# Kernel optimization log

Hardware: AMD Instinct MI355X
Metric: run time of the kernel (lower is better)

The kernel has to match this reference:

```python
import jax, jax.numpy as jnp
import numpy as np

B, N, D = 256, 131072, 256
TEMP = 0.05
EPS_SM = 1e-6
EPS_LOG = 1e-6
NUM_CLUSTERS = 1000


def _l2norm(x):
    return x / jnp.linalg.norm(x, axis=-1, keepdims=True)


def setup_inputs() -> dict:
    key = jax.random.key(0)
    k1, k2, k3, k4, k5 = jax.random.split(key, 5)
    # re-ID features are L2-normalized in practice; keeps exp(logits/temp) finite
    inputs = _l2norm(jax.random.normal(k1, (B, D), jnp.float32))
    indexes = jax.random.randint(k2, (B,), 0, N)
    labels = jax.random.randint(k3, (N,), 0, NUM_CLUSTERS)  # pseudo cluster ids buffer
    cluster_features = _l2norm(jax.random.normal(k4, (N, D), jnp.float32))
    instance_features = _l2norm(jax.random.normal(k5, (N, D), jnp.float32))
    return {
        "inputs": inputs,
        "cluster_features": cluster_features,
        "instance_features": instance_features,
        "indexes": indexes,
        "labels": labels,
    }


def reference(inputs, cluster_features, instance_features, indexes, labels):
    # targets = labels[indexes]
    targets = labels[indexes]
    # bank similarity GEMM, temperature scaling
    logits = jnp.matmul(inputs, cluster_features.T) / TEMP  # [B, N]
    # module's custom softmax: exp / (sum + eps)  (intentionally no max-subtract)
    exps = jnp.exp(logits)
    masked_sim = exps / (jnp.sum(exps, axis=1, keepdims=True) + EPS_SM)
    logp = jnp.log(masked_sim + EPS_LOG)
    # F.nll_loss: mean of -logp at target column
    loss = -jnp.mean(jnp.take_along_axis(logp, targets[:, None], axis=1))
    return loss
```

## Files before the change

kernel.cpp:

```cpp
#include <hip/hip_runtime.h>
#include <hip/hip_bf16.h>
#include <cstdint>

#define B_ 256
#define N_ 131072
#define D_ 256
#define INV_TEMP 20.0f
#define EPS_SM 1e-6f
#define EPS_LOG 1e-6f

#define TPB 512
#define BN 128
#define BK 64
#define TILES 4
#define LDB 72
#define BUFE (BN * LDB)
#define NSLOT 32

typedef __bf16 bf16_t;
typedef bf16_t bf16x8 __attribute__((ext_vector_type(8)));
typedef float f32x4 __attribute__((ext_vector_type(4)));

__device__ inline ushort f2bf(float f) {
  uint32_t u = __builtin_bit_cast(uint32_t, f);
  u += 0x7FFFu + ((u >> 16) & 1u);
  return (ushort)(u >> 16);
}

__global__ __launch_bounds__(TPB, 2)
void gemm_rowsum(const float* __restrict__ inp, const float* __restrict__ cf,
                 float* __restrict__ rowsum) {
  __shared__ ushort smem[2 * BUFE];
  const int tid  = threadIdx.x;
  const int wave = tid >> 6;
  const int lane = tid & 63;
  const int m15  = lane & 15;
  const int q    = lane >> 4;

  bf16x8 areg[8][2];
#pragma unroll
  for (int kc = 0; kc < 4; ++kc) {
    const int row = tid >> 1, half = tid & 1;
    const float* src = inp + row * D_ + kc * BK + half * 32;
#pragma unroll
    for (int i = 0; i < 8; ++i) {
      const float4 v = *(const float4*)(src + i * 4);
      ushort4 w = {f2bf(v.x), f2bf(v.y), f2bf(v.z), f2bf(v.w)};
      *(ushort4*)(&smem[row * LDB + half * 32 + i * 4]) = w;
    }
    __syncthreads();
#pragma unroll
    for (int mb = 0; mb < 2; ++mb)
#pragma unroll
      for (int ks = 0; ks < 2; ++ks)
        areg[kc * 2 + ks][mb] = __builtin_bit_cast(
            bf16x8, *(const uint4*)(&smem[(wave * 32 + mb * 16 + m15) * LDB + ks * 32 + q * 8]));
    __syncthreads();
  }

  const size_t nbase = (size_t)blockIdx.x * (TILES * BN);
  const int brow = tid >> 2, bcg = tid & 3;

  f32x4 acc[2][8];
  float rs[2][4];
#pragma unroll
  for (int mb = 0; mb < 2; ++mb) {
#pragma unroll
    for (int nb = 0; nb < 8; ++nb) acc[mb][nb] = (f32x4){0.f, 0.f, 0.f, 0.f};
#pragma unroll
    for (int r = 0; r < 4; ++r) rs[mb][r] = 0.f;
  }

  float4 ldbuf[2][4];
#define LDADDR(c) (cf + (nbase + (size_t)((c) >> 2) * BN + brow) * D_ + ((c) & 3) * BK + bcg * 16)

#pragma unroll
  for (int i = 0; i < 4; ++i) ldbuf[0][i] = *(const float4*)(LDADDR(0) + i * 4);
#pragma unroll
  for (int i = 0; i < 4; ++i) ldbuf[1][i] = *(const float4*)(LDADDR(1) + i * 4);
  {
    ushort* dst = &smem[0 * BUFE + brow * LDB + bcg * 16];
#pragma unroll
    for (int i = 0; i < 4; ++i) {
      const float4 v = ldbuf[0][i];
      ushort4 w = {f2bf(v.x), f2bf(v.y), f2bf(v.z), f2bf(v.w)};
      *(ushort4*)(dst + i * 4) = w;
    }
  }

#pragma unroll
  for (int c = 0; c < TILES * 4; ++c) {
    __syncthreads();
    if (c + 2 < TILES * 4) {
#pragma unroll
      for (int i = 0; i < 4; ++i) ldbuf[c & 1][i] = *(const float4*)(LDADDR(c + 2) + i * 4);
    }
    const ushort* bs = &smem[(c & 1) * BUFE];
#pragma unroll
    for (int ks = 0; ks < 2; ++ks) {
      bf16x8 bfr[8];
#pragma unroll
      for (int nb = 0; nb < 8; ++nb)
        bfr[nb] = __builtin_bit_cast(
            bf16x8, *(const uint4*)(&bs[(nb * 16 + m15) * LDB + ks * 32 + q * 8]));
#pragma unroll
      for (int mb = 0; mb < 2; ++mb)
#pragma unroll
        for (int nb = 0; nb < 8; ++nb)
          acc[mb][nb] = __builtin_amdgcn_mfma_f32_16x16x32_bf16(
              areg[(c & 3) * 2 + ks][mb], bfr[nb], acc[mb][nb], 0, 0, 0);
    }
    if ((c & 3) == 3) {
#pragma unroll
      for (int mb = 0; mb < 2; ++mb)
#pragma unroll
        for (int nb = 0; nb < 8; ++nb)
#pragma unroll
          for (int r = 0; r < 4; ++r)
            rs[mb][r] += __expf(acc[mb][nb][r] * INV_TEMP);
      if (c + 1 < TILES * 4) {
#pragma unroll
        for (int mb = 0; mb < 2; ++mb)
#pragma unroll
          for (int nb = 0; nb < 8; ++nb) acc[mb][nb] = (f32x4){0.f, 0.f, 0.f, 0.f};
      }
    }
    if (c + 1 < TILES * 4) {
      ushort* dst = &smem[((c + 1) & 1) * BUFE + brow * LDB + bcg * 16];
#pragma unroll
      for (int i = 0; i < 4; ++i) {
        const float4 v = ldbuf[(c + 1) & 1][i];
        ushort4 w = {f2bf(v.x), f2bf(v.y), f2bf(v.z), f2bf(v.w)};
        *(ushort4*)(dst + i * 4) = w;
      }
    }
  }

#pragma unroll
  for (int off = 8; off >= 1; off >>= 1)
#pragma unroll
    for (int mb = 0; mb < 2; ++mb)
#pragma unroll
      for (int r = 0; r < 4; ++r)
        rs[mb][r] += __shfl_xor(rs[mb][r], off, 64);

  if (m15 == 0) {
    float* slot = rowsum + (blockIdx.x & (NSLOT - 1)) * B_;
#pragma unroll
    for (int mb = 0; mb < 2; ++mb)
#pragma unroll
      for (int r = 0; r < 4; ++r)
        atomicAdd(&slot[wave * 32 + mb * 16 + q * 4 + r], rs[mb][r]);
  }
#undef LDADDR
}

__global__ __launch_bounds__(1024)
void finalize_loss(const float* __restrict__ inp, const float* __restrict__ cf,
                   const int* __restrict__ idx, const int* __restrict__ lab,
                   const float* __restrict__ rowsum, float* __restrict__ out) {
  __shared__ float red[1024];
  __shared__ float lg[256];
  const int tid = threadIdx.x;
  const int b = tid >> 2, part = tid & 3;
  const int t = lab[idx[b]];
  const float4* a = (const float4*)(inp + b * D_ + part * 64);
  const float4* c = (const float4*)(cf + (size_t)t * D_ + part * 64);
  float dot = 0.f;
#pragma unroll
  for (int i = 0; i < 16; ++i) {
    const float4 x = a[i], y = c[i];
    dot += x.x * y.x + x.y * y.y + x.z * y.z + x.w * y.w;
  }
  red[tid] = dot;
  __syncthreads();
  if (tid < 256) {
    const float d = red[tid * 4] + red[tid * 4 + 1] + red[tid * 4 + 2] + red[tid * 4 + 3];
    float S = 0.f;
#pragma unroll
    for (int s = 0; s < NSLOT; ++s) S += rowsum[s * B_ + tid];
    lg[tid] = __logf(__expf(d * INV_TEMP) / (S + EPS_SM) + EPS_LOG);
  }
  __syncthreads();
  for (int off = 128; off >= 1; off >>= 1) {
    if (tid < off) lg[tid] += lg[tid + off];
    __syncthreads();
  }
  if (tid == 0) out[0] = -lg[0] * (1.0f / 256.0f);
}

extern "C" void kernel_launch(void* const* d_in, const int* in_sizes, int n_in,
                              void* d_out, int out_size, void* d_ws, size_t ws_size,
                              hipStream_t stream) {
  const float* inp = (const float*)d_in[0];
  const float* cf  = (const float*)d_in[1];
  const int* idx = (const int*)d_in[3];
  const int* lab = (const int*)d_in[4];
  float* out = (float*)d_out;
  float* rowsum = (float*)d_ws;

  hipMemsetAsync(rowsum, 0, NSLOT * B_ * sizeof(float), stream);
  gemm_rowsum<<<dim3(N_ / (TILES * BN)), dim3(TPB), 0, stream>>>(inp, cf, rowsum);
  finalize_loss<<<dim3(1), dim3(1024), 0, stream>>>(inp, cf, idx, lab, rowsum, out);
}
```

Baseline: 288.1 us.

## Fuse loss finalization into GEMM kernel via last-block atomic counter

Removes the separate single-block finalize kernel by having the last GEMM block to finish, detected with an agent-scope atomic counter, compute the target dot products and the loss. The A operand is now loaded straight from global memory into registers instead of being staged through shared memory with barriers, and the first B tile loads are issued before it. This saves one kernel launch and the smem staging prologue, but adds a threadfence and atomic per block and a serial tail step in one block.

```diff
diff --git a/kernel.cpp b/kernel.cpp
--- a/kernel.cpp
+++ b/kernel.cpp
@@ -16,6 +16,7 @@
 #define LDB 72
 #define BUFE (BN * LDB)
 #define NSLOT 32
+#define NBLK (N_ / (TILES * BN))
 
 typedef __bf16 bf16_t;
 typedef bf16_t bf16x8 __attribute__((ext_vector_type(8)));
@@ -27,39 +28,46 @@
   return (ushort)(u >> 16);
 }
 
+struct alignas(16) U8 { ushort u[8]; };
+
 __global__ __launch_bounds__(TPB, 2)
-void gemm_rowsum(const float* __restrict__ inp, const float* __restrict__ cf,
-                 float* __restrict__ rowsum) {
+void gemm_rowsum_fused(const float* __restrict__ inp, const float* __restrict__ cf,
+                       const int* __restrict__ idx, const int* __restrict__ lab,
+                       float* __restrict__ rowsum, unsigned* __restrict__ counter,
+                       float* __restrict__ out) {
   __shared__ ushort smem[2 * BUFE];
+  __shared__ unsigned done;
   const int tid  = threadIdx.x;
   const int wave = tid >> 6;
   const int lane = tid & 63;
   const int m15  = lane & 15;
   const int q    = lane >> 4;
 
-  bf16x8 areg[8][2];
-#pragma unroll
-  for (int kc = 0; kc < 4; ++kc) {
-    const int row = tid >> 1, half = tid & 1;
-    const float* src = inp + row * D_ + kc * BK + half * 32;
-#pragma unroll
-    for (int i = 0; i < 8; ++i) {
-      const float4 v = *(const float4*)(src + i * 4);
-      ushort4 w = {f2bf(v.x), f2bf(v.y), f2bf(v.z), f2bf(v.w)};
-      *(ushort4*)(&smem[row * LDB + half * 32 + i * 4]) = w;
-    }
-    __syncthreads();
-#pragma unroll
-    for (int mb = 0; mb < 2; ++mb)
-#pragma unroll
-      for (int ks = 0; ks < 2; ++ks)
-        areg[kc * 2 + ks][mb] = __builtin_bit_cast(
-            bf16x8, *(const uint4*)(&smem[(wave * 32 + mb * 16 + m15) * LDB + ks * 32 + q * 8]));
-    __syncthreads();
-  }
-
   const size_t nbase = (size_t)blockIdx.x * (TILES * BN);
   const int brow = tid >> 2, bcg = tid & 3;
+#define LDADDR(c) (cf + (nbase + (size_t)((c) >> 2) * BN + brow) * D_ + ((c) & 3) * BK + bcg * 16)
+
+  float4 ldbuf[2][4];
+#pragma unroll
+  for (int i = 0; i < 4; ++i) ldbuf[0][i] = *(const float4*)(LDADDR(0) + i * 4);
+#pragma unroll
+  for (int i = 0; i < 4; ++i) ldbuf[1][i] = *(const float4*)(LDADDR(1) + i * 4);
+
+  bf16x8 areg[8][2];
+#pragma unroll
+  for (int kc = 0; kc < 4; ++kc)
+#pragma unroll
+    for (int ks = 0; ks < 2; ++ks)
+#pragma unroll
+      for (int mb = 0; mb < 2; ++mb) {
+        const float* s = inp + (wave * 32 + mb * 16 + m15) * D_ + kc * BK + ks * 32 + q * 8;
+        const float4 v0 = *(const float4*)s;
+        const float4 v1 = *(const float4*)(s + 4);
+        U8 t;
+        t.u[0] = f2bf(v0.x); t.u[1] = f2bf(v0.y); t.u[2] = f2bf(v0.z); t.u[3] = f2bf(v0.w);
+        t.u[4] = f2bf(v1.x); t.u[5] = f2bf(v1.y); t.u[6] = f2bf(v1.z); t.u[7] = f2bf(v1.w);
+        areg[kc * 2 + ks][mb] = __builtin_bit_cast(bf16x8, t);
+      }
 
   f32x4 acc[2][8];
   float rs[2][4];
@@ -71,20 +79,14 @@
     for (int r = 0; r < 4; ++r) rs[mb][r] = 0.f;
   }
 
-  float4 ldbuf[2][4];
-#define LDADDR(c) (cf + (nbase + (size_t)((c) >> 2) * BN + brow) * D_ + ((c) & 3) * BK + bcg * 16)
-
-#pragma unroll
-  for (int i = 0; i < 4; ++i) ldbuf[0][i] = *(const float4*)(LDADDR(0) + i * 4);
-#pragma unroll
-  for (int i = 0; i < 4; ++i) ldbuf[1][i] = *(const float4*)(LDADDR(1) + i * 4);
   {
-    ushort* dst = &smem[0 * BUFE + brow * LDB + bcg * 16];
+    ushort* dst = &smem[brow * LDB + bcg * 16];
 #pragma unroll
     for (int i = 0; i < 4; ++i) {
       const float4 v = ldbuf[0][i];
-      ushort4 w = {f2bf(v.x), f2bf(v.y), f2bf(v.z), f2bf(v.w)};
-      *(ushort4*)(dst + i * 4) = w;
+      U8 w;
+      w.u[0] = f2bf(v.x); w.u[1] = f2bf(v.y); w.u[2] = f2bf(v.z); w.u[3] = f2bf(v.w);
+      *(ushort4*)(dst + i * 4) = *(const ushort4*)&w.u[0];
     }
   }
 
@@ -130,8 +132,9 @@
 #pragma unroll
       for (int i = 0; i < 4; ++i) {
         const float4 v = ldbuf[(c + 1) & 1][i];
-        ushort4 w = {f2bf(v.x), f2bf(v.y), f2bf(v.z), f2bf(v.w)};
-        *(ushort4*)(dst + i * 4) = w;
+        U8 w;
+        w.u[0] = f2bf(v.x); w.u[1] = f2bf(v.y); w.u[2] = f2bf(v.z); w.u[3] = f2bf(v.w);
+        *(ushort4*)(dst + i * 4) = *(const ushort4*)&w.u[0];
       }
     }
   }
@@ -153,40 +156,46 @@
         atomicAdd(&slot[wave * 32 + mb * 16 + q * 4 + r], rs[mb][r]);
   }
 #undef LDADDR
-}
-
-__global__ __launch_bounds__(1024)
-void finalize_loss(const float* __restrict__ inp, const float* __restrict__ cf,
-                   const int* __restrict__ idx, const int* __restrict__ lab,
-                   const float* __restrict__ rowsum, float* __restrict__ out) {
-  __shared__ float red[1024];
-  __shared__ float lg[256];
-  const int tid = threadIdx.x;
-  const int b = tid >> 2, part = tid & 3;
-  const int t = lab[idx[b]];
-  const float4* a = (const float4*)(inp + b * D_ + part * 64);
-  const float4* c = (const float4*)(cf + (size_t)t * D_ + part * 64);
-  float dot = 0.f;
-#pragma unroll
-  for (int i = 0; i < 16; ++i) {
-    const float4 x = a[i], y = c[i];
-    dot += x.x * y.x + x.y * y.y + x.z * y.z + x.w * y.w;
-  }
-  red[tid] = dot;
+
   __syncthreads();
-  if (tid < 256) {
-    const float d = red[tid * 4] + red[tid * 4 + 1] + red[tid * 4 + 2] + red[tid * 4 + 3];
-    float S = 0.f;
-#pragma unroll
-    for (int s = 0; s < NSLOT; ++s) S += rowsum[s * B_ + tid];
-    lg[tid] = __logf(__expf(d * INV_TEMP) / (S + EPS_SM) + EPS_LOG);
+  if (tid == 0) {
+    __threadfence();
+    const unsigned prev = __hip_atomic_fetch_add(counter, 1u, __ATOMIC_ACQ_REL,
+                                                 __HIP_MEMORY_SCOPE_AGENT);
+    done = (prev == (unsigned)(gridDim.x - 1)) ? 1u : 0u;
   }
   __syncthreads();
-  for (int off = 128; off >= 1; off >>= 1) {
-    if (tid < off) lg[tid] += lg[tid + off];
+  if (done) {
+    __threadfence();
+    float* red = (float*)smem;
+    const int b = tid >> 1, part = tid & 1;
+    const int t = lab[idx[b]];
+    const float4* a4 = (const float4*)(inp + b * D_ + part * 128);
+    const float4* c4 = (const float4*)(cf + (size_t)t * D_ + part * 128);
+    float dot = 0.f;
+#pragma unroll
+    for (int i = 0; i < 32; ++i) {
+      const float4 x = a4[i], y = c4[i];
+      dot += x.x * y.x + x.y * y.y + x.z * y.z + x.w * y.w;
+    }
+    red[tid] = dot;
     __syncthreads();
-  }
-  if (tid == 0) out[0] = -lg[0] * (1.0f / 256.0f);
+    if (tid < 256) {
+      const float d = red[2 * tid] + red[2 * tid + 1];
+      float S = 0.f;
+#pragma unroll
+      for (int s = 0; s < NSLOT; ++s)
+        S += __hip_atomic_load(&rowsum[s * B_ + tid], __ATOMIC_RELAXED,
+                               __HIP_MEMORY_SCOPE_AGENT);
+      red[512 + tid] = __logf(__expf(d * INV_TEMP) / (S + EPS_SM) + EPS_LOG);
+    }
+    __syncthreads();
+    for (int off = 128; off >= 1; off >>= 1) {
+      if (tid < off) red[512 + tid] += red[512 + tid + off];
+      __syncthreads();
+    }
+    if (tid == 0) out[0] = -red[512] * (1.0f / 256.0f);
+  }
 }
 
 extern "C" void kernel_launch(void* const* d_in, const int* in_sizes, int n_in,
@@ -198,8 +207,9 @@
   const int* lab = (const int*)d_in[4];
   float* out = (float*)d_out;
   float* rowsum = (float*)d_ws;
-
-  hipMemsetAsync(rowsum, 0, NSLOT * B_ * sizeof(float), stream);
-  gemm_rowsum<<<dim3(N_ / (TILES * BN)), dim3(TPB), 0, stream>>>(inp, cf, rowsum);
-  finalize_loss<<<dim3(1), dim3(1024), 0, stream>>>(inp, cf, idx, lab, rowsum, out);
+  unsigned* counter = (unsigned*)(rowsum + NSLOT * B_);
+
+  hipMemsetAsync(d_ws, 0, (NSLOT * B_ + 16) * sizeof(float), stream);
+  gemm_rowsum_fused<<<dim3(NBLK), dim3(TPB), 0, stream>>>(inp, cf, idx, lab,
+                                                          rowsum, counter, out);
 }
```

Result: no change. 292.8 us (+1.6%).
